# Performance work log

Measured on AMD Instinct MI355X. Metric: run time of the kernel, lower is better.

## Reference

```python
import jax, jax.numpy as jnp
import numpy as np
from jax import lax

IMG = 512            # image H = W
FH = FW = 32         # feature map spatial size
A = 9                # anchors per location (3 sizes x 3 ratios)
N = FH * FW * A      # total anchors = 9216
IOU_THR = 0.7
MIN_SCORE = 0.5
MIN_SIZE = 1e-3


def make_anchors():
    """Anchors in centroid format (cx, cy, w, h), ordered (H, W, A)."""
    stride = IMG / FH
    sizes = np.array([32.0, 64.0, 128.0])
    ratios = np.array([0.5, 1.0, 2.0])
    ws = (sizes[:, None] / np.sqrt(ratios)[None, :]).reshape(-1)  # (A,)
    hs = (sizes[:, None] * np.sqrt(ratios)[None, :]).reshape(-1)  # (A,)
    cx = (np.arange(FW) + 0.5) * stride
    cy = (np.arange(FH) + 0.5) * stride
    CX = np.broadcast_to(cx[None, :, None], (FH, FW, A))
    CY = np.broadcast_to(cy[:, None, None], (FH, FW, A))
    Wg = np.broadcast_to(ws[None, None, :], (FH, FW, A))
    Hg = np.broadcast_to(hs[None, None, :], (FH, FW, A))
    anc = np.stack([CX, CY, Wg, Hg], axis=-1).reshape(-1, 4)
    return jnp.asarray(anc, dtype=jnp.float32)


def pairwise_iou(b):
    # b: (N,4) corners x1,y1,x2,y2
    x1, y1, x2, y2 = b[:, 0], b[:, 1], b[:, 2], b[:, 3]
    area = (x2 - x1) * (y2 - y1)
    ix1 = jnp.maximum(x1[:, None], x1[None, :])
    iy1 = jnp.maximum(y1[:, None], y1[None, :])
    ix2 = jnp.minimum(x2[:, None], x2[None, :])
    iy2 = jnp.minimum(y2[:, None], y2[None, :])
    inter = jnp.maximum(ix2 - ix1, 0.0) * jnp.maximum(iy2 - iy1, 0.0)
    union = area[:, None] + area[None, :] - inter
    return inter / jnp.maximum(union, 1e-9)


def nms_keep(boxes, scores, valid):
    """Greedy NMS. Returns bool keep mask of shape (N,). Index decisions only."""
    s = jnp.where(valid, scores, -jnp.inf)
    order = jnp.argsort(-s)
    b = boxes[order]
    v = valid[order]
    ious = pairwise_iou(b)  # (N, N)
    idx = jnp.arange(N)

    def body(i, supp):
        keep_i = (~supp[i]) & v[i]
        return supp | (keep_i & (ious[i] > IOU_THR) & (idx > i))

    supp = lax.fori_loop(0, N, body, jnp.zeros(N, dtype=bool))
    keep_sorted = (~supp) & v
    return jnp.zeros(N, dtype=bool).at[order].set(keep_sorted)


def setup_inputs() -> dict:
    key = jax.random.key(0)
    ks = jax.random.split(key, 4)
    return {
        "feature_map": jax.random.normal(ks[0], (1, 256, FH, FW), jnp.float32),
        "conv1_w": jax.random.normal(ks[1], (512, 256, 3, 3), jnp.float32) * 0.02,
        "conv1_b": jnp.zeros((512,), jnp.float32),
        "conv2_w": jax.random.normal(ks[2], (A, 512), jnp.float32) * 0.01,
        "conv2_b": jnp.zeros((A,), jnp.float32),
        "conv3_w": jax.random.normal(ks[3], (4 * A, 512), jnp.float32) * 0.01,
        "conv3_b": jnp.zeros((4 * A,), jnp.float32),
    }


def reference(feature_map, conv1_w, conv1_b, conv2_w, conv2_b, conv3_w, conv3_b):
    anchors = make_anchors()  # (N,4) cx,cy,w,h

    # --- conv backbone head ---
    h = lax.conv_general_dilated(
        feature_map, conv1_w, (1, 1), "SAME",
        dimension_numbers=("NCHW", "OIHW", "NCHW"))
    h = jax.nn.relu(h + conv1_b[None, :, None, None])  # (1,512,H,W)

    scores = jax.nn.sigmoid(
        jnp.einsum("bchw,ac->bahw", h, conv2_w) + conv2_b[None, :, None, None])
    scores = scores.transpose(0, 2, 3, 1).reshape(-1)  # (N,) ordered (H,W,A)

    off = jnp.einsum("bchw,oc->bohw", h, conv3_w) + conv3_b[None, :, None, None]
    off = off.reshape(1, A, 4, FH, FW).transpose(0, 3, 4, 1, 2).reshape(-1, 4)

    acx, acy, aw, ah = anchors[:, 0], anchors[:, 1], anchors[:, 2], anchors[:, 3]
    cx = acx + off[:, 0] * aw
    cy = acy + off[:, 1] * ah
    bw = aw * jnp.exp(off[:, 2])
    bh = ah * jnp.exp(off[:, 3])
    boxes = jnp.stack([cx - bw / 2, cy - bh / 2, cx + bw / 2, cy + bh / 2], axis=1)

    # --- clip to image ---
    lo = jnp.array([0.0, 0.0, 0.0, 0.0], jnp.float32)
    hi = jnp.array([IMG, IMG, IMG, IMG], jnp.float32)
    boxes = jnp.clip(boxes, lo, hi)

    # --- remove small boxes + score threshold (as a mask, jit-safe) ---
    valid = ((boxes[:, 2] - boxes[:, 0]) >= MIN_SIZE) \
          & ((boxes[:, 3] - boxes[:, 1]) >= MIN_SIZE) \
          & (scores >= MIN_SCORE)

    # --- NMS (selection is index-based; no gradient through the decision) ---
    keep = nms_keep(lax.stop_gradient(boxes), lax.stop_gradient(scores), valid)

    out = jnp.concatenate(
        [boxes * keep[:, None].astype(boxes.dtype),
         (scores * keep.astype(scores.dtype))[:, None]], axis=1)  # (N,5)
    return out
```

## Files before the change

### kernel.cpp

```cpp
#include <hip/hip_runtime.h>
#include <math.h>

#define FHW   32
#define NA    9
#define NBOX  9216
#define C1    256
#define C2    512
#define KTOT  2304
#define KS    8
#define KCH   (KTOT / KS)
#define CAP   64
#define ECAP  16384
#define ROUNDS 96

struct AnchorWH { float w[NA]; float h[NA]; };

#define FP_OFF    0u
#define WT_OFF    1183744u
#define HP_OFF    5902336u
#define BOX_OFF   22679552u
#define SC_OFF    22827008u
#define VL_OFF    22863872u
#define DEG_OFF   22900736u
#define ADJ_OFF   22937600u
#define KEEP_OFF  24117248u
#define NV_OFF    24154112u

__global__ __launch_bounds__(256) void k_prep(const float* __restrict__ fin,
                                              float* __restrict__ Fp,
                                              unsigned int* __restrict__ deg,
                                              unsigned int* __restrict__ keepG,
                                              unsigned int* __restrict__ nv,
                                              const float* __restrict__ w1,
                                              float* __restrict__ Wt) {
    if (blockIdx.x < 1156) {
        int idx = blockIdx.x * 256 + threadIdx.x;
        if (idx < 256 * 34 * 34) {
            int c   = idx / 1156;
            int rem = idx - c * 1156;
            int yy  = rem / 34;
            int xx  = rem - yy * 34;
            float v = 0.f;
            if (yy >= 1 && yy <= 32 && xx >= 1 && xx <= 32)
                v = fin[c * 1024 + (yy - 1) * 32 + (xx - 1)];
            Fp[idx] = v;
        }
        if (idx < NBOX) { deg[idx] = 0u; keepG[idx] = 0u; }
        if (idx == 0)   *nv = 0u;
    } else {
        __shared__ float tile[32][33];
        int tb  = blockIdx.x - 1156;
        int k0  = (tb % 72) * 32;
        int oc0 = (tb / 72) * 32;
        int t   = threadIdx.x;
        int r0 = t >> 5, c = t & 31;
        #pragma unroll
        for (int i = 0; i < 4; ++i) {
            int r = r0 + 8 * i;
            tile[r][c] = w1[(oc0 + r) * KTOT + k0 + c];
        }
        __syncthreads();
        #pragma unroll
        for (int i = 0; i < 4; ++i) {
            int kk  = r0 + 8 * i;
            int k   = k0 + kk;
            int ch  = k / 9;
            int kap = k - ch * 9;
            Wt[(kap * 256 + ch) * C2 + oc0 + c] = tile[c][kk];
        }
    }
}

__global__ __launch_bounds__(256, 2) void k_gemm(const float* __restrict__ Fp,
                                                 const float* __restrict__ Wt,
                                                 float* __restrict__ hp) {
    const int id = blockIdx.x;
    const int bx = id >> 5, g = id & 31;
    const int by = g >> 3, kz = g & 7;
    const int p0  = bx * 64;
    const int oc0 = by * 128;
    const int k0b = kz * KCH;
    const int t  = threadIdx.x;
    const int ty = t >> 4, tx = t & 15;

    __shared__ float As[32][64];
    __shared__ float Bs[32][128];

    const int pp   = t & 63;
    const int kkA0 = t >> 6;
    const int kkB0 = t >> 5;
    const int c4   = (t & 31) << 2;
    const int yx   = ((p0 + pp) >> 5) * 34 + ((p0 + pp) & 31);

    float acc[4][8];
    #pragma unroll
    for (int r = 0; r < 4; ++r)
        #pragma unroll
        for (int c = 0; c < 8; ++c) acc[r][c] = 0.f;

    float  aS[8];
    float4 bS[4];

    auto LOAD = [&](int s) {
        int tap = s >> 8, c0 = s & 255;
        int dy  = (tap * 11) >> 5;
        int dx  = tap - 3 * dy;
        const float* ab = Fp + (c0 * 34 + dy) * 34 + dx + yx;
        #pragma unroll
        for (int i = 0; i < 8; ++i) aS[i] = ab[(kkA0 + 4 * i) * 1156];
        const float* bb = Wt + (s + kkB0) * C2 + oc0 + c4;
        #pragma unroll
        for (int i = 0; i < 4; ++i) bS[i] = *(const float4*)(bb + (8 * i) * C2);
    };

    LOAD(k0b);
    #pragma unroll 1
    for (int kt = 0; kt < KCH; kt += 32) {
        __syncthreads();
        #pragma unroll
        for (int i = 0; i < 8; ++i) As[kkA0 + 4 * i][pp] = aS[i];
        #pragma unroll
        for (int i = 0; i < 4; ++i) *(float4*)&Bs[kkB0 + 8 * i][c4] = bS[i];
        __syncthreads();
        if (kt + 32 < KCH) LOAD(k0b + kt + 32);
        #pragma unroll
        for (int kk = 0; kk < 32; ++kk) {
            float a[4], b[8];
            *(float4*)&a[0] = *(const float4*)&As[kk][ty * 4];
            *(float4*)&b[0] = *(const float4*)&Bs[kk][tx * 4];
            *(float4*)&b[4] = *(const float4*)&Bs[kk][tx * 4 + 64];
            #pragma unroll
            for (int r = 0; r < 4; ++r)
                #pragma unroll
                for (int c = 0; c < 8; ++c) acc[r][c] += a[r] * b[c];
        }
    }
    #pragma unroll
    for (int r = 0; r < 4; ++r) {
        int p = p0 + ty * 4 + r;
        float* dst = hp + ((kz * 1024 + p) * C2 + oc0 + tx * 4);
        *(float4*)dst        = *(float4*)&acc[r][0];
        *(float4*)(dst + 64) = *(float4*)&acc[r][4];
    }
}

__global__ __launch_bounds__(256) void k_heads(const float* __restrict__ hp,
                                               const float* __restrict__ b1,
                                               const float* __restrict__ w2,
                                               const float* __restrict__ b2,
                                               const float* __restrict__ w3,
                                               const float* __restrict__ b3,
                                               float* __restrict__ boxes,
                                               float* __restrict__ scoresG,
                                               unsigned int* __restrict__ nv,
                                               unsigned int* __restrict__ vlist,
                                               AnchorWH awh) {
    const int p0 = blockIdx.x * 4;
    const int t  = threadIdx.x;
    __shared__ float hrow[4][C2];
    __shared__ float arr[4][45];

    #pragma unroll
    for (int px = 0; px < 4; ++px) {
        int p = p0 + px;
        #pragma unroll
        for (int i = 0; i < 2; ++i) {
            int c = t + 256 * i;
            float s = b1[c];
            #pragma unroll
            for (int ks = 0; ks < KS; ++ks) s += hp[(ks * 1024 + p) * C2 + c];
            hrow[px][c] = fmaxf(s, 0.f);
        }
    }
    __syncthreads();

    const int w = t >> 6, lane = t & 63;
    for (int job = w; job < 180; job += 4) {
        int px = job / 45, j = job - px * 45;
        const float* wp = (j < 9) ? (w2 + j * C2) : (w3 + (j - 9) * C2);
        float s = 0.f;
        #pragma unroll
        for (int i = 0; i < 8; ++i) s += hrow[px][lane + 64 * i] * wp[lane + 64 * i];
        #pragma unroll
        for (int d = 1; d < 64; d <<= 1) s += __shfl_xor(s, d, 64);
        if (lane == 0) arr[px][j] = s;
    }
    __syncthreads();

    if (t < 36) {
        int px = t / 9, a = t - px * 9;
        int p = p0 + px;
        float logit = arr[px][a] + b2[a];
        float score = 1.f / (1.f + expf(-logit));
        float o0 = arr[px][9 + a * 4 + 0] + b3[a * 4 + 0];
        float o1 = arr[px][9 + a * 4 + 1] + b3[a * 4 + 1];
        float o2 = arr[px][9 + a * 4 + 2] + b3[a * 4 + 2];
        float o3 = arr[px][9 + a * 4 + 3] + b3[a * 4 + 3];
        int y = p >> 5, x = p & 31;
        float ax = (x + 0.5f) * 16.f, ay = (y + 0.5f) * 16.f;
        float aw = awh.w[a], ah = awh.h[a];
        float cx = ax + o0 * aw;
        float cy = ay + o1 * ah;
        float bw = aw * expf(o2);
        float bh = ah * expf(o3);
        float x1 = fminf(fmaxf(cx - bw * 0.5f, 0.f), 512.f);
        float y1 = fminf(fmaxf(cy - bh * 0.5f, 0.f), 512.f);
        float x2 = fminf(fmaxf(cx + bw * 0.5f, 0.f), 512.f);
        float y2 = fminf(fmaxf(cy + bh * 0.5f, 0.f), 512.f);
        int n = p * 9 + a;
        float4 bx4; bx4.x = x1; bx4.y = y1; bx4.z = x2; bx4.w = y2;
        ((float4*)boxes)[n] = bx4;
        scoresG[n] = score;
        bool valid = (x2 - x1 >= 0.001f) && (y2 - y1 >= 0.001f) && (score >= 0.5f);
        if (valid) {
            unsigned int ci = atomicAdd(nv, 1u);
            vlist[ci] = (unsigned int)n;
        }
    }
}

__global__ __launch_bounds__(256) void k_adj(const unsigned int* __restrict__ nvp,
                                             const unsigned int* __restrict__ vlist,
                                             const float* __restrict__ boxes,
                                             const float* __restrict__ scoresG,
                                             unsigned int* __restrict__ deg,
                                             unsigned short* __restrict__ adj) {
    const int Nv = (int)*nvp;
    int b = blockIdx.x;
    int tv = (int)(sqrtf(2.f * b + 0.25f) - 0.5f);
    while ((tv + 1) * (tv + 2) / 2 <= b) tv++;
    while (tv * (tv + 1) / 2 > b) tv--;
    int tu = b - tv * (tv + 1) / 2;
    if (tv * 128 >= Nv) return;

    __shared__ float4 ub[128], vb[128];
    __shared__ float  us[128], vs[128];
    __shared__ int    uo[128], vo[128];
    int t = threadIdx.x;
    if (t < 128) {
        int gi = tu * 128 + t;
        if (gi < Nv) { int n = (int)vlist[gi]; ub[t] = ((const float4*)boxes)[n]; us[t] = scoresG[n]; uo[t] = n; }
        else us[t] = -1.f;
    } else {
        int tt = t - 128;
        int gj = tv * 128 + tt;
        if (gj < Nv) { int n = (int)vlist[gj]; vb[tt] = ((const float4*)boxes)[n]; vs[tt] = scoresG[n]; vo[tt] = n; }
        else vs[tt] = -1.f;
    }
    __syncthreads();

    for (int s = 0; s < 64; ++s) {
        int q  = t + 256 * s;
        int i  = q >> 7, jj = q & 127;
        if (tu == tv && i >= jj) continue;
        float su = us[i], sv = vs[jj];
        if (su < 0.f || sv < 0.f) continue;
        float4 bu = ub[i], bv = vb[jj];
        float au = (bu.z - bu.x) * (bu.w - bu.y);
        float av = (bv.z - bv.x) * (bv.w - bv.y);
        float ix1 = fmaxf(bu.x, bv.x), iy1 = fmaxf(bu.y, bv.y);
        float ix2 = fminf(bu.z, bv.z), iy2 = fminf(bu.w, bv.w);
        float inter = fmaxf(ix2 - ix1, 0.f) * fmaxf(iy2 - iy1, 0.f);
        float uni = au + av - inter;
        float iou = inter / fmaxf(uni, 1e-9f);
        if (iou > 0.7f) {
            int gi = tu * 128 + i, gj = tv * 128 + jj;
            bool uHigh = (su > sv) || (su == sv && uo[i] < vo[jj]);
            int lower = uHigh ? gj : gi;
            int upper = uHigh ? gi : gj;
            unsigned int slot = atomicAdd(&deg[lower], 1u);
            if (slot < CAP) adj[lower * CAP + slot] = (unsigned short)upper;
        }
    }
}

__global__ __launch_bounds__(512) void k_peel(const unsigned int* __restrict__ nvp,
                                              const unsigned int* __restrict__ vlist,
                                              const unsigned int* __restrict__ degG,
                                              const unsigned short* __restrict__ adjG,
                                              unsigned int* __restrict__ keepG) {
    __shared__ unsigned short offL[NBOX + 2];
    __shared__ unsigned char  st[NBOX];
    __shared__ unsigned short csr[ECAP];
    __shared__ unsigned int   scratch[512];
    __shared__ unsigned char  flags[ROUNDS];
    const int t  = threadIdx.x;
    const int Nv = (int)*nvp;
    const int chunk = (Nv + 511) / 512;
    const int i0 = t * chunk;
    const int i1 = (i0 + chunk < Nv) ? (i0 + chunk) : Nv;

    if (t < ROUNDS) flags[t] = 0;

    unsigned int lsum = 0;
    for (int i = i0; i < i1; ++i) {
        unsigned int d = degG[i];
        if (d > CAP) d = CAP;
        st[i] = (unsigned char)d;
        lsum += d;
    }
    scratch[t] = lsum;
    __syncthreads();
    for (int ofs = 1; ofs < 512; ofs <<= 1) {
        unsigned int v = (t >= ofs) ? scratch[t - ofs] : 0u;
        __syncthreads();
        scratch[t] += v;
        __syncthreads();
    }
    if (t == 511) {
        unsigned int tot = scratch[511];
        offL[Nv] = (unsigned short)(tot < ECAP ? tot : ECAP);
    }
    unsigned int amask = 0;
    {
        unsigned int off = scratch[t] - lsum;
        for (int i = i0; i < i1; ++i) {
            unsigned int o = (off < ECAP) ? off : ECAP;
            offL[i] = (unsigned short)o;
            int d = st[i];
            int ld = (int)ECAP - (int)o; if (ld > d) ld = d; if (ld < 0) ld = 0;
            for (int s = 0; s < ld; ++s)
                csr[o + s] = adjG[i * CAP + s];
            off += d;
            if (d == 0) st[i] = 1;
            else { st[i] = 0; amask |= 1u << (i - i0); }
        }
    }
    __syncthreads();

    for (int r = 0; r < ROUNDS; ++r) {
        bool any = false;
        unsigned int m = amask;
        while (m) {
            int b = __ffs(m) - 1; m &= m - 1;
            int i = i0 + b;
            int o = offL[i], on = offL[i + 1];
            int d, ld;
            if (on < ECAP) { d = on - o; ld = d; }
            else {
            unsigned int dg = degG[i]; d = (dg > CAP) ? CAP : (int)dg;
                ld = (int)ECAP - o; if (ld < 0) ld = 0; if (ld > d) ld = d;
            }
            bool kseen = false, useen = false;
            for (int s = 0; s < d; ++s) {
                int j = (s < ld) ? (int)csr[o + s] : (int)adjG[i * CAP + s];
                unsigned char v = st[j];
                kseen |= (v == 1);
                useen |= (v == 0);
            }
            if (kseen)       { st[i] = 2; any = true; amask &= ~(1u << b); }
            else if (!useen) { st[i] = 1; any = true; amask &= ~(1u << b); }
        }
        if (any) flags[r] = 1;
        __syncthreads();
        if (!flags[r]) break;
    }

    for (int i = i0; i < i1; ++i)
        if (st[i] == 1) keepG[vlist[i]] = 1u;
}

__global__ __launch_bounds__(256) void k_out(const float* __restrict__ boxes,
                                             const float* __restrict__ scoresG,
                                             const unsigned int* __restrict__ keepG,
                                             float* __restrict__ out) {
    int n = blockIdx.x * 256 + threadIdx.x;
    if (n >= NBOX) return;
    float k = keepG[n] ? 1.f : 0.f;
    float4 b = ((const float4*)boxes)[n];
    out[n * 5 + 0] = b.x * k;
    out[n * 5 + 1] = b.y * k;
    out[n * 5 + 2] = b.z * k;
    out[n * 5 + 3] = b.w * k;
    out[n * 5 + 4] = scoresG[n] * k;
}

extern "C" void kernel_launch(void* const* d_in, const int* in_sizes, int n_in,
                              void* d_out, int out_size, void* d_ws, size_t ws_size,
                              hipStream_t stream) {
    const float* fin = (const float*)d_in[0];
    const float* w1  = (const float*)d_in[1];
    const float* b1  = (const float*)d_in[2];
    const float* w2  = (const float*)d_in[3];
    const float* b2  = (const float*)d_in[4];
    const float* w3  = (const float*)d_in[5];
    const float* b3  = (const float*)d_in[6];
    float* out = (float*)d_out;

    char* ws = (char*)d_ws;
    float*          Fp    = (float*)(ws + FP_OFF);
    float*          Wt    = (float*)(ws + WT_OFF);
    float*          hp    = (float*)(ws + HP_OFF);
    float*          boxes = (float*)(ws + BOX_OFF);
    float*          sc    = (float*)(ws + SC_OFF);
    unsigned int*   vlist = (unsigned int*)(ws + VL_OFF);
    unsigned int*   deg   = (unsigned int*)(ws + DEG_OFF);
    unsigned short* adj   = (unsigned short*)(ws + ADJ_OFF);
    unsigned int*   keepG = (unsigned int*)(ws + KEEP_OFF);
    unsigned int*   nv    = (unsigned int*)(ws + NV_OFF);

    AnchorWH awh;
    {
        const double sizes[3]  = {32.0, 64.0, 128.0};
        const double ratios[3] = {0.5, 1.0, 2.0};
        for (int si = 0; si < 3; ++si)
            for (int ri = 0; ri < 3; ++ri) {
                awh.w[si * 3 + ri] = (float)(sizes[si] / sqrt(ratios[ri]));
                awh.h[si * 3 + ri] = (float)(sizes[si] * sqrt(ratios[ri]));
            }
    }

    k_prep<<<dim3(1156 + 72 * 16), 256, 0, stream>>>(fin, Fp, deg, keepG, nv, w1, Wt);
    k_gemm<<<dim3(512), 256, 0, stream>>>(Fp, Wt, hp);
    k_heads<<<dim3(256), 256, 0, stream>>>(hp, b1, w2, b2, w3, b3, boxes, sc, nv, vlist, awh);
    k_adj<<<dim3(72 * 73 / 2), 256, 0, stream>>>(nv, vlist, boxes, sc, deg, adj);
    k_peel<<<dim3(1), 512, 0, stream>>>(nv, vlist, deg, adj, keepG);
    k_out<<<dim3((NBOX + 255) / 256), 256, 0, stream>>>(boxes, sc, keepG, out);
}
```

Baseline: 203.5 us.

## Widen GEMM tiles with double-buffered LDS, fuse output into peel, grow CSR cap

```diff
diff --git a/kernel.cpp b/kernel.cpp
--- a/kernel.cpp
+++ b/kernel.cpp
@@ -9,8 +9,10 @@
 #define KTOT  2304
 #define KS    8
 #define KCH   (KTOT / KS)
+#define BK    32
+#define NTILES (KCH / BK)
 #define CAP   64
-#define ECAP  16384
+#define ECAP  32768
 #define ROUNDS 96
 
 struct AnchorWH { float w[NA]; float h[NA]; };
@@ -23,16 +25,15 @@
 #define VL_OFF    22863872u
 #define DEG_OFF   22900736u
 #define ADJ_OFF   22937600u
-#define KEEP_OFF  24117248u
 #define NV_OFF    24154112u
 
 __global__ __launch_bounds__(256) void k_prep(const float* __restrict__ fin,
                                               float* __restrict__ Fp,
                                               unsigned int* __restrict__ deg,
-                                              unsigned int* __restrict__ keepG,
                                               unsigned int* __restrict__ nv,
                                               const float* __restrict__ w1,
-                                              float* __restrict__ Wt) {
+                                              float* __restrict__ Wt,
+                                              float* __restrict__ out) {
     if (blockIdx.x < 1156) {
         int idx = blockIdx.x * 256 + threadIdx.x;
         if (idx < 256 * 34 * 34) {
@@ -45,8 +46,9 @@
                 v = fin[c * 1024 + (yy - 1) * 32 + (xx - 1)];
             Fp[idx] = v;
         }
-        if (idx < NBOX) { deg[idx] = 0u; keepG[idx] = 0u; }
-        if (idx == 0)   *nv = 0u;
+        if (idx < NBOX)     deg[idx] = 0u;
+        if (idx < NBOX * 5) out[idx] = 0.f;
+        if (idx == 0)       *nv = 0u;
     } else {
         __shared__ float tile[32][33];
         int tb  = blockIdx.x - 1156;
@@ -71,35 +73,35 @@
     }
 }
 
-__global__ __launch_bounds__(256, 2) void k_gemm(const float* __restrict__ Fp,
+__global__ __launch_bounds__(256, 1) void k_gemm(const float* __restrict__ Fp,
                                                  const float* __restrict__ Wt,
                                                  float* __restrict__ hp) {
     const int id = blockIdx.x;
-    const int bx = id >> 5, g = id & 31;
+    const int bx = id >> 4, g = id & 15;
     const int by = g >> 3, kz = g & 7;
     const int p0  = bx * 64;
-    const int oc0 = by * 128;
+    const int oc0 = by * 256;
     const int k0b = kz * KCH;
     const int t  = threadIdx.x;
-    const int ty = t >> 4, tx = t & 15;
-
-    __shared__ float As[32][64];
-    __shared__ float Bs[32][128];
+    const int ty = t >> 5, tx = t & 31;
+
+    __shared__ float As[2][BK][64];
+    __shared__ float Bs[2][BK][260];
 
     const int pp   = t & 63;
     const int kkA0 = t >> 6;
-    const int kkB0 = t >> 5;
-    const int c4   = (t & 31) << 2;
+    const int rB   = t >> 3;
+    const int cB   = t & 7;
     const int yx   = ((p0 + pp) >> 5) * 34 + ((p0 + pp) & 31);
 
-    float acc[4][8];
+    float accL[8][4], accR[8][4];
     #pragma unroll
-    for (int r = 0; r < 4; ++r)
-        #pragma unroll
-        for (int c = 0; c < 8; ++c) acc[r][c] = 0.f;
+    for (int r = 0; r < 8; ++r)
+        #pragma unroll
+        for (int c = 0; c < 4; ++c) { accL[r][c] = 0.f; accR[r][c] = 0.f; }
 
     float  aS[8];
-    float4 bS[4];
+    float4 bS[8];
 
     auto LOAD = [&](int s) {
         int tap = s >> 8, c0 = s & 255;
@@ -108,39 +110,52 @@
         const float* ab = Fp + (c0 * 34 + dy) * 34 + dx + yx;
         #pragma unroll
         for (int i = 0; i < 8; ++i) aS[i] = ab[(kkA0 + 4 * i) * 1156];
-        const float* bb = Wt + (s + kkB0) * C2 + oc0 + c4;
-        #pragma unroll
-        for (int i = 0; i < 4; ++i) bS[i] = *(const float4*)(bb + (8 * i) * C2);
+        const float* bb = Wt + (s + rB) * C2 + oc0 + cB * 4;
+        #pragma unroll
+        for (int i = 0; i < 8; ++i) bS[i] = *(const float4*)(bb + 32 * i);
     };
+    auto STORE = [&](int buf) {
+        #pragma unroll
+        for (int i = 0; i < 8; ++i) As[buf][kkA0 + 4 * i][pp] = aS[i];
+        #pragma unroll
+        for (int i = 0; i < 8; ++i) *(float4*)&Bs[buf][rB][cB * 4 + 32 * i] = bS[i];
+    };
 
     LOAD(k0b);
+    STORE(0);
+    __syncthreads();
+
     #pragma unroll 1
-    for (int kt = 0; kt < KCH; kt += 32) {
-        __syncthreads();
-        #pragma unroll
-        for (int i = 0; i < 8; ++i) As[kkA0 + 4 * i][pp] = aS[i];
-        #pragma unroll
-        for (int i = 0; i < 4; ++i) *(float4*)&Bs[kkB0 + 8 * i][c4] = bS[i];
-        __syncthreads();
-        if (kt + 32 < KCH) LOAD(k0b + kt + 32);
-        #pragma unroll
-        for (int kk = 0; kk < 32; ++kk) {
-            float a[4], b[8];
-            *(float4*)&a[0] = *(const float4*)&As[kk][ty * 4];
-            *(float4*)&b[0] = *(const float4*)&Bs[kk][tx * 4];
-            *(float4*)&b[4] = *(const float4*)&Bs[kk][tx * 4 + 64];
+    for (int tile = 0; tile < NTILES; ++tile) {
+        const int cur = tile & 1;
+        if (tile + 1 < NTILES) LOAD(k0b + (tile + 1) * BK);
+        #pragma unroll
+        for (int kk = 0; kk < BK; ++kk) {
+            float a[8], bl[4], br[4];
+            *(float4*)&a[0]  = *(const float4*)&As[cur][kk][ty * 8];
+            *(float4*)&a[4]  = *(const float4*)&As[cur][kk][ty * 8 + 4];
+            *(float4*)&bl[0] = *(const float4*)&Bs[cur][kk][tx * 4];
+            *(float4*)&br[0] = *(const float4*)&Bs[cur][kk][128 + tx * 4];
             #pragma unroll
-            for (int r = 0; r < 4; ++r)
+            for (int r = 0; r < 8; ++r)
                 #pragma unroll
-                for (int c = 0; c < 8; ++c) acc[r][c] += a[r] * b[c];
-        }
-    }
+                for (int c = 0; c < 4; ++c) {
+                    accL[r][c] += a[r] * bl[c];
+                    accR[r][c] += a[r] * br[c];
+                }
+        }
+        if (tile + 1 < NTILES) {
+            STORE(cur ^ 1);
+            __syncthreads();
+        }
+    }
+
     #pragma unroll
-    for (int r = 0; r < 4; ++r) {
-        int p = p0 + ty * 4 + r;
+    for (int r = 0; r < 8; ++r) {
+        int p = p0 + ty * 8 + r;
         float* dst = hp + ((kz * 1024 + p) * C2 + oc0 + tx * 4);
-        *(float4*)dst        = *(float4*)&acc[r][0];
-        *(float4*)(dst + 64) = *(float4*)&acc[r][4];
+        *(float4*)dst         = *(float4*)&accL[r][0];
+        *(float4*)(dst + 128) = *(float4*)&accR[r][0];
     }
 }
 
@@ -278,7 +293,9 @@
                                               const unsigned int* __restrict__ vlist,
                                               const unsigned int* __restrict__ degG,
                                               const unsigned short* __restrict__ adjG,
-                                              unsigned int* __restrict__ keepG) {
+                                              const float* __restrict__ boxes,
+                                              const float* __restrict__ scoresG,
+                                              float* __restrict__ out) {
     __shared__ unsigned short offL[NBOX + 2];
     __shared__ unsigned char  st[NBOX];
     __shared__ unsigned short csr[ECAP];
@@ -338,7 +355,7 @@
             int d, ld;
             if (on < ECAP) { d = on - o; ld = d; }
             else {
-            unsigned int dg = degG[i]; d = (dg > CAP) ? CAP : (int)dg;
+                unsigned int dg = degG[i]; d = (dg > CAP) ? CAP : (int)dg;
                 ld = (int)ECAP - o; if (ld < 0) ld = 0; if (ld > d) ld = d;
             }
             bool kseen = false, useen = false;
@@ -356,23 +373,17 @@
         if (!flags[r]) break;
     }
 
-    for (int i = i0; i < i1; ++i)
-        if (st[i] == 1) keepG[vlist[i]] = 1u;
-}
-
-__global__ __launch_bounds__(256) void k_out(const float* __restrict__ boxes,
-                                             const float* __restrict__ scoresG,
-                                             const unsigned int* __restrict__ keepG,
-                                             float* __restrict__ out) {
-    int n = blockIdx.x * 256 + threadIdx.x;
-    if (n >= NBOX) return;
-    float k = keepG[n] ? 1.f : 0.f;
-    float4 b = ((const float4*)boxes)[n];
-    out[n * 5 + 0] = b.x * k;
-    out[n * 5 + 1] = b.y * k;
-    out[n * 5 + 2] = b.z * k;
-    out[n * 5 + 3] = b.w * k;
-    out[n * 5 + 4] = scoresG[n] * k;
+    for (int i = i0; i < i1; ++i) {
+        if (st[i] == 1) {
+            int n = (int)vlist[i];
+            float4 b = ((const float4*)boxes)[n];
+            out[n * 5 + 0] = b.x;
+            out[n * 5 + 1] = b.y;
+            out[n * 5 + 2] = b.z;
+            out[n * 5 + 3] = b.w;
+            out[n * 5 + 4] = scoresG[n];
+        }
+    }
 }
 
 extern "C" void kernel_launch(void* const* d_in, const int* in_sizes, int n_in,
@@ -396,7 +407,6 @@
     unsigned int*   vlist = (unsigned int*)(ws + VL_OFF);
     unsigned int*   deg   = (unsigned int*)(ws + DEG_OFF);
     unsigned short* adj   = (unsigned short*)(ws + ADJ_OFF);
-    unsigned int*   keepG = (unsigned int*)(ws + KEEP_OFF);
     unsigned int*   nv    = (unsigned int*)(ws + NV_OFF);
 
     AnchorWH awh;
@@ -410,10 +420,9 @@
             }
     }
 
-    k_prep<<<dim3(1156 + 72 * 16), 256, 0, stream>>>(fin, Fp, deg, keepG, nv, w1, Wt);
-    k_gemm<<<dim3(512), 256, 0, stream>>>(Fp, Wt, hp);
+    k_prep<<<dim3(1156 + 72 * 16), 256, 0, stream>>>(fin, Fp, deg, nv, w1, Wt, out);
+    k_gemm<<<dim3(256), 256, 0, stream>>>(Fp, Wt, hp);
     k_heads<<<dim3(256), 256, 0, stream>>>(hp, b1, w2, b2, w3, b3, boxes, sc, nv, vlist, awh);
     k_adj<<<dim3(72 * 73 / 2), 256, 0, stream>>>(nv, vlist, boxes, sc, deg, adj);
-    k_peel<<<dim3(1), 512, 0, stream>>>(nv, vlist, deg, adj, keepG);
-    k_out<<<dim3((NBOX + 255) / 256), 256, 0, stream>>>(boxes, sc, keepG, out);
-}
+    k_peel<<<dim3(1), 512, 0, stream>>>(nv, vlist, deg, adj, boxes, sc, out);
+}
```

After: 316.5 us. +55.5%, slower.
